# Performance work log

Hardware: AMD Instinct MI355X
Metric: run time of the kernel (lower is better)

Reference implementation:

```python
import jax, jax.numpy as jnp
import numpy as np

BATCH, T, S, M = 512, 4096, 64, 125  # batch, seq_len, n_states, emission alphabet (5^3)


def setup_inputs() -> dict:
    key = jax.random.key(0)
    k1, k2, k3, k4 = jax.random.split(key, 4)
    obs = jax.random.randint(k1, (BATCH, T), 0, M)
    x = jax.nn.one_hot(obs, M, dtype=jnp.float32)            # [B, T, M] one-hot emissions
    I = jax.nn.softmax(jax.random.normal(k2, (1, S)))        # initial state distribution [1, S]
    A = jax.nn.softmax(jax.random.normal(k3, (S, S)), axis=-1)   # transition matrix, rows sum to 1
    Bm = jax.nn.softmax(jax.random.normal(k4, (M, S)), axis=0)   # emission matrix, cols sum to 1
    return {"x": x, "I": I, "A": A, "Bm": Bm}


def reference(x, I, A, Bm):
    """HMM forward algorithm with per-step normalization (default scaling branch of CgpHmmCell).

    Returns the accumulated log-likelihood [B, 1].
    """
    xT = jnp.swapaxes(x, 0, 1)  # [T, B, M] for scan over time

    # t = 1: R = I (broadcast over batch), old_loglik = 0
    E0 = xT[0] @ Bm                                  # [B, S]
    u0 = E0 * I                                      # unscaled alpha
    Z0 = jnp.sum(u0, axis=1, keepdims=True)          # [B, 1]
    carry0 = (u0 / Z0, jnp.log(Z0))

    def step(carry, x_t):
        alpha, ll = carry
        R = alpha @ A                                # [B, S] transition
        E = x_t @ Bm                                 # [B, S] emission lookup (one-hot matmul)
        u = E * R
        Z = jnp.sum(u, axis=1, keepdims=True)        # per-sequence scaling factor
        return (u / Z, ll + jnp.log(Z)), None

    (alpha, loglik), _ = jax.lax.scan(step, carry0, xT[1:])
    return loglik
```

## Files before the change

### kernel.cpp

```cpp
#include <hip/hip_runtime.h>


#define BATCH 512
#define T 4096
#define S 64
#define M 125
#define CHUNKP 4
#define BURNP 2
#define NPACK (CHUNKP + BURNP)
#define WPB 8
#define BSTR 68
#define WSTR 20

typedef __attribute__((ext_vector_type(8))) short bf16x8;
typedef __attribute__((ext_vector_type(4))) float f32x4;

union BFU { unsigned u[4]; bf16x8 v; };

__device__ __forceinline__ unsigned pk_trunc(float a, float b) {
    return (__float_as_uint(b) & 0xFFFF0000u) | (__float_as_uint(a) >> 16);
}
__device__ __forceinline__ unsigned pk_rne(float a, float b) {
    unsigned ua = __float_as_uint(a); ua += 0x7FFFu + ((ua >> 16) & 1u);
    unsigned ub = __float_as_uint(b); ub += 0x7FFFu + ((ub >> 16) & 1u);
    return (ub & 0xFFFF0000u) | (ua >> 16);
}

__global__ __launch_bounds__(256) void extract_obs(const float4* __restrict__ x4,
                                                   unsigned char* __restrict__ obs) {
    const long long n4 = (long long)BATCH * T * M / 4;
    long long stride = (long long)gridDim.x * blockDim.x;
    for (long long i = (long long)blockIdx.x * blockDim.x + threadIdx.x; i < n4; i += stride) {
        float4 v = x4[i];
        if (v.x != 0.0f || v.y != 0.0f || v.z != 0.0f || v.w != 0.0f) {
            long long e = i * 4;
            if (v.x != 0.0f) { long long r = (e + 0) / M; obs[r] = (unsigned char)(e + 0 - r * M); }
            if (v.y != 0.0f) { long long r = (e + 1) / M; obs[r] = (unsigned char)(e + 1 - r * M); }
            if (v.z != 0.0f) { long long r = (e + 2) / M; obs[r] = (unsigned char)(e + 2 - r * M); }
            if (v.w != 0.0f) { long long r = (e + 3) / M; obs[r] = (unsigned char)(e + 3 - r * M); }
        }
    }
}

__global__ __launch_bounds__(512, 4) void hmm_mfma(const unsigned char* __restrict__ obs,
                                                   const float* __restrict__ Iv,
                                                   const float* __restrict__ A,
                                                   const float* __restrict__ Bm,
                                                   float* __restrict__ out) {
    __shared__ __align__(16) float BmL[M * BSTR];
    __shared__ __align__(16) float ILds[S];
    __shared__ unsigned wscAll[WPB][32 * WSTR];

    const int tid = threadIdx.x, wv = tid >> 6, lane = tid & 63;
    const int s = lane & 15, g = lane >> 4;

    for (int i = tid; i < M * S; i += WPB * 64) BmL[(i >> 6) * BSTR + (i & 63)] = Bm[i];
    if (tid < S) ILds[tid] = Iv[tid];
    __syncthreads();

    BFU Af[4][2];
#pragma unroll
    for (int mt = 0; mt < 4; ++mt)
#pragma unroll
        for (int kf = 0; kf < 2; ++kf)
#pragma unroll
            for (int j2 = 0; j2 < 4; ++j2) {
                int k0 = kf * 32 + g * 8 + 2 * j2;
                Af[mt][kf].u[j2] = pk_rne(A[(size_t)k0 * S + mt * 16 + s],
                                          A[(size_t)(k0 + 1) * S + mt * 16 + s]);
            }

    const int W = blockIdx.x * WPB + wv;
    const int seq = W >> 3, hw = W & 7;
    const int chunk = hw * 16 + s;
    const bool c0wave = (hw == 0);
    const bool is_c0 = c0wave && (s == 0);

    const unsigned long long* orow = (const unsigned long long*)(obs + (size_t)seq * T);
    const int idx0 = chunk * CHUNKP - BURNP;

    unsigned* wsc = wscAll[wv];

    BFU Bf[2];
#pragma unroll
    for (int kf = 0; kf < 2; ++kf)
#pragma unroll
        for (int j = 0; j < 4; ++j) Bf[kf].u[j] = 0x3F803F80u;

    float w[4][4];
    float Ls = 0.f, S0v = 0.f, c = 1.f;

    int i0 = idx0 < 0 ? 0 : idx0;
    unsigned long long u = orow[i0];

    for (int p = 0; p < NPACK; ++p) {
        int in_ = idx0 + p + 1;
        in_ = in_ < 0 ? 0 : (in_ > T / 8 - 1 ? T / 8 - 1 : in_);
        unsigned long long un = orow[in_];
        const bool ovp = c0wave && (p == BURNP);
#pragma unroll
        for (int k = 0; k < 8; ++k) {
            const int o = (int)((u >> (8 * k)) & 255ull);
            f32x4 E[4];
#pragma unroll
            for (int mt = 0; mt < 4; ++mt)
                E[mt] = *(const f32x4*)&BmL[o * BSTR + mt * 16 + g * 4];
            f32x4 acc[4];
#pragma unroll
            for (int mt = 0; mt < 4; ++mt) {
                f32x4 z = {0.f, 0.f, 0.f, 0.f};
                z = __builtin_amdgcn_mfma_f32_16x16x32_bf16(Af[mt][0].v, Bf[0].v, z, 0, 0, 0);
                acc[mt] = __builtin_amdgcn_mfma_f32_16x16x32_bf16(Af[mt][1].v, Bf[1].v, z, 0, 0, 0);
            }
#pragma unroll
            for (int mt = 0; mt < 4; ++mt)
#pragma unroll
                for (int r = 0; r < 4; ++r) {
                    float wv_ = acc[mt][r] * E[mt][r];
                    if (ovp && k == 0)
                        wv_ = is_c0 ? ILds[mt * 16 + g * 4 + r] * E[mt][r] : wv_;
                    w[mt][r] = wv_;
                }
            float scale = 1.f;
            if (k == 7) {
                c = __uint_as_float(__builtin_amdgcn_ds_bpermute(s << 2, __float_as_uint(w[0][0])));
                c = fmaxf(c, 1e-37f);
                Ls += __log2f(c);
                scale = __builtin_amdgcn_rcpf(c);
            }
#pragma unroll
            for (int mt = 0; mt < 4; ++mt)
#pragma unroll
                for (int pr = 0; pr < 2; ++pr) {
                    float v0 = w[mt][2 * pr], v1 = w[mt][2 * pr + 1];
                    if (k == 7) { v0 *= scale; v1 *= scale; }
                    wsc[(2 * g + pr + 8 * mt) * WSTR + s] = pk_trunc(v0, v1);
                }
#pragma unroll
            for (int kf = 0; kf < 2; ++kf)
#pragma unroll
                for (int j = 0; j < 4; ++j)
                    Bf[kf].u[j] = wsc[(4 * g + j + 16 * kf) * WSTR + s];
        }
        if (p == BURNP - 1) {
            float sw = 0.f;
#pragma unroll
            for (int mt = 0; mt < 4; ++mt)
#pragma unroll
                for (int r = 0; r < 4; ++r) sw += w[mt][r];
            sw += __shfl_xor(sw, 16);
            sw += __shfl_xor(sw, 32);
            S0v = (chunk == 0) ? Ls : (Ls + __log2f(sw) - __log2f(c));
        }
        u = un;
    }

    float sw = 0.f;
#pragma unroll
    for (int mt = 0; mt < 4; ++mt)
#pragma unroll
        for (int r = 0; r < 4; ++r) sw += w[mt][r];
    sw += __shfl_xor(sw, 16);
    sw += __shfl_xor(sw, 32);
    float Lfin = Ls + __log2f(sw) - __log2f(c) - S0v;
    if (lane < 16)
        atomicAdd(out + seq, Lfin * 0.6931471805599453f);
}

extern "C" void kernel_launch(void* const* d_in, const int* in_sizes, int n_in,
                              void* d_out, int out_size, void* d_ws, size_t ws_size,
                              hipStream_t stream) {
    const float* x  = (const float*)d_in[0];
    const float* I  = (const float*)d_in[1];
    const float* A  = (const float*)d_in[2];
    const float* Bm = (const float*)d_in[3];
    float* out = (float*)d_out;
    unsigned char* obs = (unsigned char*)d_ws;

    hipMemsetAsync(out, 0, (size_t)out_size * sizeof(float), stream);
    extract_obs<<<65536, 256, 0, stream>>>((const float4*)x, obs);
    hmm_mfma<<<(BATCH * 8) / WPB, WPB * 64, 0, stream>>>(obs, I, A, Bm, out);
}
```

Measured before the change: 1.367 ms.

## Interleave four independent chunks per wave and vectorize LDS exchange

Each wave now processes four independent sequence chunks in an interleaved loop instead of one, cutting the grid from 512 to 256 blocks of 4 waves. The goal is to hide MFMA and LDS latency through independent dependency chains within a wave rather than relying on many waves. The LDS scratch layout for repacking alpha into MFMA operands is changed to 128-bit stores, the padded emission table is dropped, and partial log-likelihoods are reduced in-wave so only one atomic is issued per wave. The cost is higher register pressure and fewer resident waves.

```diff
diff --git a/kernel.cpp b/kernel.cpp
--- a/kernel.cpp
+++ b/kernel.cpp
@@ -7,13 +7,13 @@
 #define M 125
 #define CHUNKP 4
 #define BURNP 2
-#define NPACK (CHUNKP + BURNP)
-#define WPB 8
-#define BSTR 68
-#define WSTR 20
+#define NPACK 6
+#define WPB 4
+#define NQ 4
 
 typedef __attribute__((ext_vector_type(8))) short bf16x8;
 typedef __attribute__((ext_vector_type(4))) float f32x4;
+typedef __attribute__((ext_vector_type(4))) unsigned u32x4;
 
 union BFU { unsigned u[4]; bf16x8 v; };
 
@@ -42,19 +42,19 @@
     }
 }
 
-__global__ __launch_bounds__(512, 4) void hmm_mfma(const unsigned char* __restrict__ obs,
-                                                   const float* __restrict__ Iv,
-                                                   const float* __restrict__ A,
-                                                   const float* __restrict__ Bm,
-                                                   float* __restrict__ out) {
-    __shared__ __align__(16) float BmL[M * BSTR];
+__global__ __launch_bounds__(256) void hmm_mfma(const unsigned char* __restrict__ obs,
+                                                const float* __restrict__ Iv,
+                                                const float* __restrict__ A,
+                                                const float* __restrict__ Bm,
+                                                float* __restrict__ out) {
+    __shared__ __align__(16) float BmL[M * S];
     __shared__ __align__(16) float ILds[S];
-    __shared__ unsigned wscAll[WPB][32 * WSTR];
+    __shared__ u32x4 wscAll[WPB][64 * 3];
 
     const int tid = threadIdx.x, wv = tid >> 6, lane = tid & 63;
     const int s = lane & 15, g = lane >> 4;
 
-    for (int i = tid; i < M * S; i += WPB * 64) BmL[(i >> 6) * BSTR + (i & 63)] = Bm[i];
+    for (int i = tid; i < M * S; i += WPB * 64) BmL[i] = Bm[i];
     if (tid < S) ILds[tid] = Iv[tid];
     __syncthreads();
 
@@ -71,100 +71,125 @@
             }
 
     const int W = blockIdx.x * WPB + wv;
-    const int seq = W >> 3, hw = W & 7;
-    const int chunk = hw * 16 + s;
-    const bool c0wave = (hw == 0);
-    const bool is_c0 = c0wave && (s == 0);
-
+    const int seq = W >> 1, half = W & 1;
     const unsigned long long* orow = (const unsigned long long*)(obs + (size_t)seq * T);
-    const int idx0 = chunk * CHUNKP - BURNP;
-
-    unsigned* wsc = wscAll[wv];
-
-    BFU Bf[2];
-#pragma unroll
-    for (int kf = 0; kf < 2; ++kf)
-#pragma unroll
-        for (int j = 0; j < 4; ++j) Bf[kf].u[j] = 0x3F803F80u;
-
-    float w[4][4];
-    float Ls = 0.f, S0v = 0.f, c = 1.f;
-
-    int i0 = idx0 < 0 ? 0 : idx0;
-    unsigned long long u = orow[i0];
+    unsigned* wsc = (unsigned*)wscAll[wv];
+
+    const int wbase = lane * 12;
+    int rbase[2];
+#pragma unroll
+    for (int a = 0; a < 2; ++a) {
+        int t = 2 * g + a;
+        rbase[a] = (s + 16 * (t & 3)) * 12 + (t >> 2) * 2;
+    }
+
+    int idx0[NQ];
+    unsigned long long u[NQ], un[NQ];
+    BFU Bf[NQ][2];
+    float Ls[NQ], S0v[NQ], cc[NQ], swv[NQ];
+#pragma unroll
+    for (int q = 0; q < NQ; ++q) {
+        int chunk = half * 64 + q * 16 + s;
+        idx0[q] = chunk * CHUNKP - BURNP;
+        u[q] = orow[idx0[q] < 0 ? 0 : idx0[q]];
+        Ls[q] = 0.f; S0v[q] = 0.f; cc[q] = 1.f; swv[q] = 1.f;
+#pragma unroll
+        for (int kf = 0; kf < 2; ++kf)
+#pragma unroll
+            for (int j = 0; j < 4; ++j) Bf[q][kf].u[j] = 0x3F803F80u;
+    }
 
     for (int p = 0; p < NPACK; ++p) {
-        int in_ = idx0 + p + 1;
-        in_ = in_ < 0 ? 0 : (in_ > T / 8 - 1 ? T / 8 - 1 : in_);
-        unsigned long long un = orow[in_];
-        const bool ovp = c0wave && (p == BURNP);
+#pragma unroll
+        for (int q = 0; q < NQ; ++q) {
+            int in_ = idx0[q] + p + 1;
+            in_ = in_ < 0 ? 0 : (in_ > T / 8 - 1 ? T / 8 - 1 : in_);
+            un[q] = orow[in_];
+        }
+        const bool ovp = (half == 0) && (p == BURNP);
 #pragma unroll
         for (int k = 0; k < 8; ++k) {
-            const int o = (int)((u >> (8 * k)) & 255ull);
-            f32x4 E[4];
-#pragma unroll
-            for (int mt = 0; mt < 4; ++mt)
-                E[mt] = *(const f32x4*)&BmL[o * BSTR + mt * 16 + g * 4];
-            f32x4 acc[4];
-#pragma unroll
-            for (int mt = 0; mt < 4; ++mt) {
-                f32x4 z = {0.f, 0.f, 0.f, 0.f};
-                z = __builtin_amdgcn_mfma_f32_16x16x32_bf16(Af[mt][0].v, Bf[0].v, z, 0, 0, 0);
-                acc[mt] = __builtin_amdgcn_mfma_f32_16x16x32_bf16(Af[mt][1].v, Bf[1].v, z, 0, 0, 0);
+#pragma unroll
+            for (int q = 0; q < NQ; ++q) {
+                const int o = (int)((u[q] >> (8 * k)) & 255ull);
+                const float* br = &BmL[o << 6];
+                f32x4 E[4];
+#pragma unroll
+                for (int mt = 0; mt < 4; ++mt)
+                    E[mt] = *(const f32x4*)&br[mt * 16 + g * 4];
+                float w[4][4];
+#pragma unroll
+                for (int mt = 0; mt < 4; ++mt) {
+                    f32x4 z = {0.f, 0.f, 0.f, 0.f};
+                    z = __builtin_amdgcn_mfma_f32_16x16x32_bf16(Af[mt][0].v, Bf[q][0].v, z, 0, 0, 0);
+                    z = __builtin_amdgcn_mfma_f32_16x16x32_bf16(Af[mt][1].v, Bf[q][1].v, z, 0, 0, 0);
+#pragma unroll
+                    for (int r = 0; r < 4; ++r) w[mt][r] = z[r] * E[mt][r];
+                }
+                if (ovp && k == 0 && q == 0) {
+                    const bool c0 = (s == 0);
+#pragma unroll
+                    for (int mt = 0; mt < 4; ++mt)
+#pragma unroll
+                        for (int r = 0; r < 4; ++r)
+                            w[mt][r] = c0 ? ILds[mt * 16 + g * 4 + r] * E[mt][r] : w[mt][r];
+                }
+                float scale = 1.f;
+                if (k == 7) {
+                    float swl = 0.f;
+#pragma unroll
+                    for (int mt = 0; mt < 4; ++mt)
+#pragma unroll
+                        for (int r = 0; r < 4; ++r) swl += w[mt][r];
+                    swl += __shfl_xor(swl, 16);
+                    swl += __shfl_xor(swl, 32);
+                    swv[q] = swl;
+                    float c = __uint_as_float(__builtin_amdgcn_ds_bpermute(s << 2, __float_as_uint(w[0][0])));
+                    c = fmaxf(c, 1e-37f);
+                    cc[q] = c;
+                    Ls[q] += __log2f(c);
+                    scale = __builtin_amdgcn_rcpf(c);
+                }
+                unsigned P[8];
+#pragma unroll
+                for (int mt = 0; mt < 4; ++mt)
+#pragma unroll
+                    for (int pr = 0; pr < 2; ++pr) {
+                        float v0 = w[mt][2 * pr], v1 = w[mt][2 * pr + 1];
+                        if (k == 7) { v0 *= scale; v1 *= scale; }
+                        P[mt * 2 + pr] = pk_trunc(v0, v1);
+                    }
+                u32x4 w0 = {P[0], P[1], P[2], P[3]}, w1 = {P[4], P[5], P[6], P[7]};
+                *(u32x4*)&wsc[wbase] = w0;
+                *(u32x4*)&wsc[wbase + 4] = w1;
+#pragma unroll
+                for (int kf = 0; kf < 2; ++kf)
+#pragma unroll
+                    for (int j2 = 0; j2 < 4; ++j2)
+                        Bf[q][kf].u[j2] = wsc[rbase[j2 >> 1] + 4 * kf + (j2 & 1)];
             }
-#pragma unroll
-            for (int mt = 0; mt < 4; ++mt)
-#pragma unroll
-                for (int r = 0; r < 4; ++r) {
-                    float wv_ = acc[mt][r] * E[mt][r];
-                    if (ovp && k == 0)
-                        wv_ = is_c0 ? ILds[mt * 16 + g * 4 + r] * E[mt][r] : wv_;
-                    w[mt][r] = wv_;
-                }
-            float scale = 1.f;
-            if (k == 7) {
-                c = __uint_as_float(__builtin_amdgcn_ds_bpermute(s << 2, __float_as_uint(w[0][0])));
-                c = fmaxf(c, 1e-37f);
-                Ls += __log2f(c);
-                scale = __builtin_amdgcn_rcpf(c);
+        }
+        if (p == BURNP - 1) {
+#pragma unroll
+            for (int q = 0; q < NQ; ++q) {
+                const bool ch0 = (half == 0) && (q == 0) && (s == 0);
+                S0v[q] = ch0 ? Ls[q] : (Ls[q] + __log2f(swv[q]) - __log2f(cc[q]));
             }
-#pragma unroll
-            for (int mt = 0; mt < 4; ++mt)
-#pragma unroll
-                for (int pr = 0; pr < 2; ++pr) {
-                    float v0 = w[mt][2 * pr], v1 = w[mt][2 * pr + 1];
-                    if (k == 7) { v0 *= scale; v1 *= scale; }
-                    wsc[(2 * g + pr + 8 * mt) * WSTR + s] = pk_trunc(v0, v1);
-                }
-#pragma unroll
-            for (int kf = 0; kf < 2; ++kf)
-#pragma unroll
-                for (int j = 0; j < 4; ++j)
-                    Bf[kf].u[j] = wsc[(4 * g + j + 16 * kf) * WSTR + s];
-        }
-        if (p == BURNP - 1) {
-            float sw = 0.f;
-#pragma unroll
-            for (int mt = 0; mt < 4; ++mt)
-#pragma unroll
-                for (int r = 0; r < 4; ++r) sw += w[mt][r];
-            sw += __shfl_xor(sw, 16);
-            sw += __shfl_xor(sw, 32);
-            S0v = (chunk == 0) ? Ls : (Ls + __log2f(sw) - __log2f(c));
-        }
-        u = un;
-    }
-
-    float sw = 0.f;
-#pragma unroll
-    for (int mt = 0; mt < 4; ++mt)
-#pragma unroll
-        for (int r = 0; r < 4; ++r) sw += w[mt][r];
-    sw += __shfl_xor(sw, 16);
-    sw += __shfl_xor(sw, 32);
-    float Lfin = Ls + __log2f(sw) - __log2f(c) - S0v;
-    if (lane < 16)
-        atomicAdd(out + seq, Lfin * 0.6931471805599453f);
+        }
+#pragma unroll
+        for (int q = 0; q < NQ; ++q) u[q] = un[q];
+    }
+
+    float tot = 0.f;
+#pragma unroll
+    for (int q = 0; q < NQ; ++q)
+        tot += Ls[q] + __log2f(swv[q]) - __log2f(cc[q]) - S0v[q];
+    tot += __shfl_xor(tot, 1);
+    tot += __shfl_xor(tot, 2);
+    tot += __shfl_xor(tot, 4);
+    tot += __shfl_xor(tot, 8);
+    if (lane == 0)
+        atomicAdd(out + seq, tot * 0.6931471805599453f);
 }
 
 extern "C" void kernel_launch(void* const* d_in, const int* in_sizes, int n_in,
@@ -179,5 +204,5 @@
 
     hipMemsetAsync(out, 0, (size_t)out_size * sizeof(float), stream);
     extract_obs<<<65536, 256, 0, stream>>>((const float4*)x, obs);
-    hmm_mfma<<<(BATCH * 8) / WPB, WPB * 64, 0, stream>>>(obs, I, A, Bm, out);
-}
+    hmm_mfma<<<256, WPB * 64, 0, stream>>>(obs, I, A, Bm, out);
+}
```

Result: no change. 1.341 ms (-1.9%).
